# Kernel optimization log

Hardware: AMD Instinct MI355X
Metric: run time of the kernel (lower is better)

Reference implementation:

```python
import jax, jax.numpy as jnp
import numpy as np

# Model constants (match init_kwargs + mamba_ssm defaults)
CIN, COUT, K, STRIDE = 64, 128, 4, 4
D = 128            # d_model = features_out
DI = 256           # d_inner = 2*D (expand=2)
NSTATE = 16        # d_state
DCONV = 4          # depthwise conv width
DT_RANK = 8        # ceil(D/16)
NB = 3             # blocks per direction
NTOT = 2 * NB      # forward + backward stacks


def setup_inputs() -> dict:
    key = jax.random.key(0)
    ks = jax.random.split(key, 10)
    s = 0.02
    x = jax.random.normal(ks[0], (2, CIN, 8192), jnp.float32)
    convd_w = jax.random.normal(ks[1], (COUT, CIN, K), jnp.float32) * s
    convd_b = jnp.zeros((COUT,), jnp.float32)
    ln_w = jnp.ones((NTOT, D), jnp.float32)
    ln_b = jnp.zeros((NTOT, D), jnp.float32)
    in_proj_w = jax.random.normal(ks[2], (NTOT, 2 * DI, D), jnp.float32) * s
    conv_w = jax.random.normal(ks[3], (NTOT, DI, DCONV), jnp.float32) * s
    conv_b = jnp.zeros((NTOT, DI), jnp.float32)
    xproj_w = jax.random.normal(ks[4], (NTOT, DT_RANK + 2 * NSTATE, DI), jnp.float32) * s
    dtproj_w = jax.random.normal(ks[5], (NTOT, DI, DT_RANK), jnp.float32) * s
    dtproj_b = jax.random.normal(ks[6], (NTOT, DI), jnp.float32) * s
    # S4D-real init: A = -[1..N]
    A_log = jnp.log(jnp.broadcast_to(jnp.arange(1, NSTATE + 1, dtype=jnp.float32), (NTOT, DI, NSTATE)))
    Dparam = jnp.ones((NTOT, DI), jnp.float32)
    outproj_w = jax.random.normal(ks[7], (NTOT, D, DI), jnp.float32) * s
    return dict(x=x, convd_w=convd_w, convd_b=convd_b, ln_w=ln_w, ln_b=ln_b,
                in_proj_w=in_proj_w, conv_w=conv_w, conv_b=conv_b, xproj_w=xproj_w,
                dtproj_w=dtproj_w, dtproj_b=dtproj_b, A_log=A_log, Dparam=Dparam,
                outproj_w=outproj_w)


def _silu(x):
    return x * jax.nn.sigmoid(x)


def _layernorm(x, w, b, eps=1e-5):
    m = x.mean(-1, keepdims=True)
    xc = x - m
    v = (xc * xc).mean(-1, keepdims=True)
    return xc * jax.lax.rsqrt(v + eps) * w + b


def _mamba_mixer(x, in_proj_w, conv_w, conv_b, xproj_w, dtproj_w, dtproj_b, A_log, Dp, outproj_w):
    # x: (B, L, D)
    B, L, _ = x.shape
    xz = jnp.einsum('bld,ed->ble', x, in_proj_w)          # (B, L, 2*DI)
    xm, z = jnp.split(xz, 2, axis=-1)
    # causal depthwise conv (pad left DCONV-1, truncate to L)
    xp = jnp.pad(xm, ((0, 0), (DCONV - 1, 0), (0, 0)))
    xc = conv_b
    acc = jnp.zeros_like(xm)
    for k in range(DCONV):
        acc = acc + xp[:, k:k + L, :] * conv_w[:, k]
    xc = _silu(acc + conv_b)                               # (B, L, DI)
    dbc = jnp.einsum('ble,ne->bln', xc, xproj_w)           # (B, L, DT_RANK + 2N)
    dt, Bc, Cc = jnp.split(dbc, [DT_RANK, DT_RANK + NSTATE], axis=-1)
    dt = jax.nn.softplus(jnp.einsum('blr,dr->bld', dt, dtproj_w) + dtproj_b)  # (B, L, DI)
    A = -jnp.exp(A_log)                                    # (DI, N)
    dA = jnp.exp(dt[..., None] * A)                        # (B, L, DI, N)
    dBx = dt[..., None] * Bc[:, :, None, :] * xc[..., None]

    def step(h, inp):
        dA_t, dBx_t, C_t = inp
        h = dA_t * h + dBx_t                               # (B, DI, N)
        y = jnp.einsum('bdn,bn->bd', h, C_t)
        return h, y

    h0 = jnp.zeros((B, DI, NSTATE), x.dtype)
    _, ys = jax.lax.scan(step, h0, (jnp.swapaxes(dA, 0, 1), jnp.swapaxes(dBx, 0, 1), jnp.swapaxes(Cc, 0, 1)))
    y = jnp.swapaxes(ys, 0, 1)                             # (B, L, DI)
    y = (y + Dp * xc) * _silu(z)
    return jnp.einsum('ble,de->bld', y, outproj_w)         # (B, L, D)


def _mamba_stack(x, off, ln_w, ln_b, in_proj_w, conv_w, conv_b, xproj_w, dtproj_w, dtproj_b, A_log, Dparam, outproj_w):
    # mamba_ssm Block semantics: residual = x (+ prev residual); x = mixer(norm(residual))
    res = None
    cur = x
    for i in range(NB):
        j = off + i
        res = cur if res is None else cur + res
        hn = _layernorm(res, ln_w[j], ln_b[j])
        cur = _mamba_mixer(hn, in_proj_w[j], conv_w[j], conv_b[j], xproj_w[j],
                           dtproj_w[j], dtproj_b[j], A_log[j], Dparam[j], outproj_w[j])
    return cur, res


def reference(x, convd_w, convd_b, ln_w, ln_b, in_proj_w, conv_w, conv_b, xproj_w,
              dtproj_w, dtproj_b, A_log, Dparam, outproj_w):
    # downsampling conv + SiLU
    y = jax.lax.conv_general_dilated(x, convd_w, (STRIDE,), 'VALID',
                                     dimension_numbers=('NCH', 'OIH', 'NCH'))
    y = _silu(y + convd_b[None, :, None])                  # (B, COUT, L')
    h = jnp.swapaxes(y, 1, 2)                              # (B, L', D)
    xf, rf = _mamba_stack(h, 0, ln_w, ln_b, in_proj_w, conv_w, conv_b, xproj_w,
                          dtproj_w, dtproj_b, A_log, Dparam, outproj_w)
    xb, rb = _mamba_stack(h[:, ::-1, :], NB, ln_w, ln_b, in_proj_w, conv_w, conv_b, xproj_w,
                          dtproj_w, dtproj_b, A_log, Dparam, outproj_w)
    out = (xf + rf) + (xb + rb)[:, ::-1, :]
    return jnp.swapaxes(out, 1, 2), rf, rb
```

## Files before the change

kernel.cpp:

```cpp
#include <hip/hip_runtime.h>
#include <hip/hip_bf16.h>
#include <math.h>

#define B    2
#define CIN  64
#define LIN  8192
#define L    2048
#define D    128
#define DI   256
#define NS   16
#define RK   8
#define NSTREAM 4
#define CH   32
#define NCH  (L/CH)
#define TOK  (NSTREAM*L)
#define SZ_D ((size_t)TOK*D)
#define SZ_DI ((size_t)TOK*DI)
#define SXM 280
#define SHN 152

typedef short  bfrag __attribute__((ext_vector_type(8)));
typedef float  facc  __attribute__((ext_vector_type(4)));
#define MFMA __builtin_amdgcn_mfma_f32_16x16x32_bf16

__device__ __forceinline__ float sigmoidf_(float x){ return 1.f/(1.f+__expf(-x)); }
__device__ __forceinline__ float siluf_(float x){ return x*sigmoidf_(x); }
__device__ __forceinline__ ushort f2bf(float f){
    unsigned u = __float_as_uint(f);
    u += 0x7fffu + ((u>>16)&1u);
    return (ushort)(u>>16);
}
__device__ __forceinline__ float bf2f(ushort u){ return __uint_as_float(((unsigned)u)<<16); }
__device__ __forceinline__ float softplusf_(float t){
    return (t > 20.f) ? t : __logf(1.f + __expf(t));
}

__global__ void k_cvtall(const float* __restrict__ cw, const float* __restrict__ ipw,
                         const float* __restrict__ opw, const float* __restrict__ xpw,
                         ushort* __restrict__ dst){
    int i = blockIdx.x*256 + threadIdx.x;
    ushort v;
    if (i < 32768)       v = f2bf(cw[i]);
    else if (i < 425984) v = f2bf(ipw[i-32768]);
    else if (i < 622592) v = f2bf(opw[i-425984]);
    else {
        int t = i - 622592;
        int k = t & 255, nr = (t>>8) & 63, j = t>>14;
        v = (nr < 40) ? f2bf(xpw[((size_t)j*40 + nr)*256 + k]) : (ushort)0;
    }
    dst[i] = v;
}

__global__ void k_down(const float* __restrict__ x, const ushort* __restrict__ wd,
                       const float* __restrict__ bias, float* __restrict__ h){
    __shared__ ushort sxd[64*SXM];
    int tid = threadIdx.x;
    int m0 = blockIdx.x*64;
    int b = m0 >> 11;
    int l0 = m0 & 2047;
    for (int idx = tid; idx < 64*64; idx += 256){
        int t = idx & 63, cc = idx >> 6;
        float4 v = *(const float4*)(x + ((size_t)(b*CIN + cc))*LIN + 4*(l0+t));
        ushort4 o; o.x=f2bf(v.x); o.y=f2bf(v.y); o.z=f2bf(v.z); o.w=f2bf(v.w);
        *(ushort4*)&sxd[t*SXM + cc*4] = o;
    }
    __syncthreads();
    int w = tid>>6, lane = tid&63, rw = w>>1, cw = w&1;
    int q = lane>>4, r = lane&15;
    int n0 = blockIdx.y*64 + cw*32;
    const ushort* b0p = wd + (size_t)(n0 + r)*256 + q*8;
    const ushort* b1p = b0p + (size_t)16*256;
    facc acc[2][2] = {};
    #pragma unroll
    for (int kb=0; kb<8; ++kb){
        bfrag a0 = *(bfrag*)&sxd[(rw*32 + r)*SXM + kb*32 + q*8];
        bfrag a1 = *(bfrag*)&sxd[(rw*32 + 16 + r)*SXM + kb*32 + q*8];
        bfrag b0 = *(const bfrag*)(b0p + kb*32);
        bfrag b1 = *(const bfrag*)(b1p + kb*32);
        acc[0][0] = MFMA(a0,b0,acc[0][0],0,0,0);
        acc[0][1] = MFMA(a0,b1,acc[0][1],0,0,0);
        acc[1][0] = MFMA(a1,b0,acc[1][0],0,0,0);
        acc[1][1] = MFMA(a1,b1,acc[1][1],0,0,0);
    }
    #pragma unroll
    for (int im=0; im<2; ++im)
    #pragma unroll
    for (int in=0; in<2; ++in){
        int col = n0 + in*16 + r;
        float bv = bias[col];
        #pragma unroll
        for (int r2=0; r2<4; ++r2){
            int row = m0 + rw*32 + im*16 + q*4 + r2;
            int bb = row >> 11, l = row & 2047;
            float v = siluf_(acc[im][in][r2] + bv);
            h[((size_t)(bb*L + l))*D + col] = v;
            h[((size_t)((2+bb)*L + (L-1-l)))*D + col] = v;
        }
    }
}

__global__ void __launch_bounds__(256,1)
k_head(const float* __restrict__ curIn, const float* __restrict__ resIn,
       float* __restrict__ resOut,
       const float* __restrict__ lnw, const float* __restrict__ lnb,
       const ushort* __restrict__ wbi, const ushort* __restrict__ wbx,
       const float* __restrict__ cw, const float* __restrict__ cb,
       const float* __restrict__ Wdt, const float* __restrict__ bdt,
       const float* __restrict__ A_log,
       float* __restrict__ z, float* __restrict__ xc,
       float* __restrict__ dtr, float* __restrict__ Bc, float* __restrict__ Cc,
       float* __restrict__ Aprod, float* __restrict__ Bend, int blk, int first){
    __shared__ ushort smHn[35*SHN];
    __shared__ ushort smXm[35*SXM];
    __shared__ ushort smXc[32*SXM];
    __shared__ float  smDbc[32*68];
    const int tid = threadIdx.x;
    const int bi = blockIdx.x;
    const int s = bi >> 6, c = bi & 63;
    const int j = (s>>1)*3 + blk;
    const int base_tok = s*L + c*CH;

    {
        int t = tid >> 3, g8 = tid & 7;
        size_t off = (size_t)(base_tok + t)*D + g8*16;
        float4 v[4];
        const float4* cp = (const float4*)(curIn + off);
        #pragma unroll
        for (int i=0;i<4;++i) v[i] = cp[i];
        if (!first){
            const float4* rp = (const float4*)(resIn + off);
            #pragma unroll
            for (int i=0;i<4;++i){ float4 rv=rp[i]; v[i].x+=rv.x; v[i].y+=rv.y; v[i].z+=rv.z; v[i].w+=rv.w; }
        }
        {
            float4* ro = (float4*)(resOut + off);
            #pragma unroll
            for (int i=0;i<4;++i) ro[i] = v[i];
        }
        float s1=0.f, s2=0.f;
        #pragma unroll
        for (int i=0;i<4;++i){
            s1 += v[i].x+v[i].y+v[i].z+v[i].w;
            s2 += v[i].x*v[i].x+v[i].y*v[i].y+v[i].z*v[i].z+v[i].w*v[i].w;
        }
        s1 += __shfl_xor(s1,1); s2 += __shfl_xor(s2,1);
        s1 += __shfl_xor(s1,2); s2 += __shfl_xor(s2,2);
        s1 += __shfl_xor(s1,4); s2 += __shfl_xor(s2,4);
        float mean = s1*(1.f/128.f);
        float var  = s2*(1.f/128.f) - mean*mean;
        float rstd = rsqrtf(var + 1e-5f);
        const float4* lwp = (const float4*)(lnw + j*D + g8*16);
        const float4* lbp = (const float4*)(lnb + j*D + g8*16);
        #pragma unroll
        for (int i=0;i<4;++i){
            float4 lw = lwp[i], lb = lbp[i];
            ushort4 o;
            o.x = f2bf((v[i].x-mean)*rstd*lw.x + lb.x);
            o.y = f2bf((v[i].y-mean)*rstd*lw.y + lb.y);
            o.z = f2bf((v[i].z-mean)*rstd*lw.z + lb.z);
            o.w = f2bf((v[i].w-mean)*rstd*lw.w + lb.w);
            *(ushort4*)&smHn[t*SHN + g8*16 + i*4] = o;
        }
    }
    if (c > 0 && tid < 24){
        int t = tid >> 3, g8 = tid & 7;
        size_t off = (size_t)(base_tok - 3 + t)*D + g8*16;
        float4 v[4];
        const float4* cp = (const float4*)(curIn + off);
        #pragma unroll
        for (int i=0;i<4;++i) v[i] = cp[i];
        if (!first){
            const float4* rp = (const float4*)(resIn + off);
            #pragma unroll
            for (int i=0;i<4;++i){ float4 rv=rp[i]; v[i].x+=rv.x; v[i].y+=rv.y; v[i].z+=rv.z; v[i].w+=rv.w; }
        }
        float s1=0.f, s2=0.f;
        #pragma unroll
        for (int i=0;i<4;++i){
            s1 += v[i].x+v[i].y+v[i].z+v[i].w;
            s2 += v[i].x*v[i].x+v[i].y*v[i].y+v[i].z*v[i].z+v[i].w*v[i].w;
        }
        s1 += __shfl_xor(s1,1); s2 += __shfl_xor(s2,1);
        s1 += __shfl_xor(s1,2); s2 += __shfl_xor(s2,2);
        s1 += __shfl_xor(s1,4); s2 += __shfl_xor(s2,4);
        float mean = s1*(1.f/128.f);
        float var  = s2*(1.f/128.f) - mean*mean;
        float rstd = rsqrtf(var + 1e-5f);
        const float4* lwp = (const float4*)(lnw + j*D + g8*16);
        const float4* lbp = (const float4*)(lnb + j*D + g8*16);
        #pragma unroll
        for (int i=0;i<4;++i){
            float4 lw = lwp[i], lb = lbp[i];
            ushort4 o;
            o.x = f2bf((v[i].x-mean)*rstd*lw.x + lb.x);
            o.y = f2bf((v[i].y-mean)*rstd*lw.y + lb.y);
            o.z = f2bf((v[i].z-mean)*rstd*lw.z + lb.z);
            o.w = f2bf((v[i].w-mean)*rstd*lw.w + lb.w);
            *(ushort4*)&smHn[(32+t)*SHN + g8*16 + i*4] = o;
        }
    }
    __syncthreads();

    {
        int w = tid>>6, lane = tid&63, q = lane>>4, r = lane&15;
        bfrag a[3][4];
        #pragma unroll
        for (int rt=0; rt<3; ++rt)
        #pragma unroll
        for (int kb=0; kb<4; ++kb)
            a[rt][kb] = *(bfrag*)&smHn[(rt*16 + r)*SHN + kb*32 + q*8];
        #pragma unroll
        for (int ct=0; ct<8; ++ct){
            int n0 = w*128 + ct*16;
            const ushort* bp = wbi + ((size_t)j*512 + n0 + r)*128 + q*8;
            facc a0 = {}, a1 = {}, a2 = {};
            #pragma unroll
            for (int kb=0; kb<4; ++kb){
                bfrag bv = *(const bfrag*)(bp + kb*32);
                a0 = MFMA(a[0][kb], bv, a0, 0,0,0);
                a1 = MFMA(a[1][kb], bv, a1, 0,0,0);
                a2 = MFMA(a[2][kb], bv, a2, 0,0,0);
            }
            int colL = n0 + r;
            if (colL < DI){
                #pragma unroll
                for (int r2=0;r2<4;++r2){
                    int rr = q*4 + r2;
                    smXm[rr*SXM + colL]      = f2bf(a0[r2]);
                    smXm[(16+rr)*SXM + colL] = f2bf(a1[r2]);
                    if (rr < 3) smXm[(32+rr)*SXM + colL] = f2bf(a2[r2]);
                }
            } else {
                int cz = colL - DI;
                #pragma unroll
                for (int r2=0;r2<4;++r2){
                    int rr = q*4 + r2;
                    z[(size_t)(base_tok + rr)*DI + cz]      = a0[r2];
                    z[(size_t)(base_tok + 16 + rr)*DI + cz] = a1[r2];
                }
            }
        }
    }
    __syncthreads();

    {
        const float* w4 = cw + ((size_t)j*DI + tid)*4;
        float cw0=w4[0], cw1=w4[1], cw2=w4[2], cw3=w4[3];
        float cbb = cb[j*DI + tid];
        float xm1=0.f, xm2=0.f, xm3=0.f;
        if (c > 0){
            xm3 = bf2f(smXm[32*SXM + tid]);
            xm2 = bf2f(smXm[33*SXM + tid]);
            xm1 = bf2f(smXm[34*SXM + tid]);
        }
        #pragma unroll 4
        for (int i=0;i<CH;++i){
            float x0 = bf2f(smXm[i*SXM + tid]);
            float v = siluf_(cbb + cw3*x0 + cw2*xm1 + cw1*xm2 + cw0*xm3);
            smXc[i*SXM + tid] = f2bf(v);
            xc[(size_t)(base_tok+i)*DI + tid] = v;
            xm3 = xm2; xm2 = xm1; xm1 = x0;
        }
    }
    __syncthreads();

    {
        int w = tid>>6, lane = tid&63, q = lane>>4, r = lane&15;
        facc a0 = {}, a1 = {};
        const ushort* bp = wbx + ((size_t)j*64 + w*16 + r)*256 + q*8;
        #pragma unroll
        for (int kb=0; kb<8; ++kb){
            bfrag av0 = *(bfrag*)&smXc[r*SXM + kb*32 + q*8];
            bfrag av1 = *(bfrag*)&smXc[(16+r)*SXM + kb*32 + q*8];
            bfrag bv  = *(const bfrag*)(bp + kb*32);
            a0 = MFMA(av0, bv, a0, 0,0,0);
            a1 = MFMA(av1, bv, a1, 0,0,0);
        }
        int col = w*16 + r;
        #pragma unroll
        for (int r2=0;r2<4;++r2){
            int rr = q*4 + r2;
            smDbc[rr*68 + col]      = a0[r2];
            smDbc[(16+rr)*68 + col] = a1[r2];
            int row0 = base_tok + rr, row1 = base_tok + 16 + rr;
            if      (col < 8){  dtr[(size_t)row0*RK + col] = a0[r2];      dtr[(size_t)row1*RK + col] = a1[r2]; }
            else if (col < 24){ Bc [(size_t)row0*NS + (col-8)] = a0[r2];  Bc [(size_t)row1*NS + (col-8)] = a1[r2]; }
            else if (col < 40){ Cc [(size_t)row0*NS + (col-24)] = a0[r2]; Cc [(size_t)row1*NS + (col-24)] = a1[r2]; }
        }
    }
    __syncthreads();

    {
        float A[NS], wv[RK];
        const float* ar = A_log + ((size_t)j*DI + tid)*NS;
        #pragma unroll
        for (int n=0;n<NS;++n) A[n] = -__expf(ar[n]);
        const float* wr = Wdt + ((size_t)j*DI + tid)*RK;
        #pragma unroll
        for (int r=0;r<RK;++r) wv[r] = wr[r];
        float bb2 = bdt[j*DI + tid];
        float ap[NS], hs[NS];
        #pragma unroll
        for (int n=0;n<NS;++n){ ap[n]=1.f; hs[n]=0.f; }
        #pragma unroll 4
        for (int l=0;l<CH;++l){
            float t = bb2;
            #pragma unroll
            for (int r=0;r<RK;++r) t += smDbc[l*68+r]*wv[r];
            float dtv = softplusf_(t);
            float xv  = bf2f(smXc[l*SXM + tid]);
            float dbx = dtv*xv;
            #pragma unroll
            for (int n=0;n<NS;++n){
                float dA = __expf(dtv*A[n]);
                ap[n] *= dA;
                hs[n] = dA*hs[n] + dbx*smDbc[l*68+8+n];
            }
        }
        size_t pb = (size_t)bi*4096 + tid;
        #pragma unroll
        for (int n=0;n<NS;++n){
            Aprod[pb + (size_t)n*256] = ap[n];
            Bend [pb + (size_t)n*256] = hs[n];
        }
    }
}

__global__ void k_scanmid(const float* __restrict__ Aprod, float* __restrict__ Bend){
    int tid = blockIdx.x*128 + threadIdx.x;
    int s = tid >> 12;
    int nd = tid & 4095;
    size_t base = (size_t)s*NCH*4096 + nd;
    float h = 0.f;
    for (int c0=0; c0<NCH; c0+=16){
        float a[16], b[16];
        #pragma unroll
        for (int i=0;i<16;++i){
            a[i] = Aprod[base + (size_t)(c0+i)*4096];
            b[i] = Bend [base + (size_t)(c0+i)*4096];
        }
        #pragma unroll
        for (int i=0;i<16;++i){
            Bend[base + (size_t)(c0+i)*4096] = h;
            h = a[i]*h + b[i];
        }
    }
}

__global__ void k_tail(const float* __restrict__ dtr, const float* __restrict__ xcv,
                       const float* __restrict__ Bc, const float* __restrict__ Cc,
                       const float* __restrict__ A_log,
                       const float* __restrict__ Wdt, const float* __restrict__ bdt,
                       const float* __restrict__ h0, const float* __restrict__ z,
                       const float* __restrict__ Dp, const ushort* __restrict__ wbo,
                       float* __restrict__ cur, int blk){
    int c = blockIdx.x, s = blockIdx.y; int j = (s>>1)*3 + blk;
    int d = threadIdx.x;
    __shared__ float sB[CH*NS], sC[CH*NS], sdtr[CH*RK];
    __shared__ ushort sg[CH*SXM];
    int base_tok = s*L + c*CH;
    sB[d] = Bc[(size_t)base_tok*NS + d];
    sB[256+d] = Bc[(size_t)base_tok*NS + 256 + d];
    sC[d] = Cc[(size_t)base_tok*NS + d];
    sC[256+d] = Cc[(size_t)base_tok*NS + 256 + d];
    sdtr[d] = dtr[(size_t)base_tok*RK + d];
    float A[NS], wv[RK];
    const float* ar = A_log + ((size_t)j*DI + d)*NS;
    #pragma unroll
    for (int n=0;n<NS;++n) A[n] = -__expf(ar[n]);
    const float* wr = Wdt + ((size_t)j*DI + d)*RK;
    #pragma unroll
    for (int r=0;r<RK;++r) wv[r] = wr[r];
    float bb = bdt[j*DI + d];
    float Dpd = Dp[j*DI + d];
    float hs[NS];
    size_t pb = (size_t)(s*NCH + c)*4096 + d;
    #pragma unroll
    for (int n=0;n<NS;++n) hs[n] = h0[pb + (size_t)n*256];
    __syncthreads();
    #pragma unroll 4
    for (int l=0;l<CH;++l){
        float t = bb;
        #pragma unroll
        for (int r=0;r<RK;++r) t += sdtr[l*RK+r]*wv[r];
        float dtv = softplusf_(t);
        float xv  = xcv[(size_t)(base_tok+l)*DI + d];
        float dbx = dtv*xv;
        float p = 0.f;
        #pragma unroll
        for (int n=0;n<NS;++n){
            float dA = __expf(dtv*A[n]);
            hs[n] = dA*hs[n] + dbx*sB[l*NS+n];
            p += hs[n]*sC[l*NS+n];
        }
        float zv = z[(size_t)(base_tok+l)*DI + d];
        sg[l*SXM + d] = f2bf((p + Dpd*xv)*siluf_(zv));
    }
    __syncthreads();
    int w = d>>6, lane = d&63, q = lane>>4, r = lane&15;
    facc acc[2][2] = {};
    const ushort* b0p = wbo + ((size_t)j*128 + w*32 + r)*256 + q*8;
    const ushort* b1p = b0p + 16*256;
    #pragma unroll
    for (int kb=0; kb<8; ++kb){
        bfrag av0 = *(bfrag*)&sg[r*SXM + kb*32 + q*8];
        bfrag av1 = *(bfrag*)&sg[(16+r)*SXM + kb*32 + q*8];
        bfrag bv0 = *(const bfrag*)(b0p + kb*32);
        bfrag bv1 = *(const bfrag*)(b1p + kb*32);
        acc[0][0] = MFMA(av0,bv0,acc[0][0],0,0,0);
        acc[0][1] = MFMA(av0,bv1,acc[0][1],0,0,0);
        acc[1][0] = MFMA(av1,bv0,acc[1][0],0,0,0);
        acc[1][1] = MFMA(av1,bv1,acc[1][1],0,0,0);
    }
    #pragma unroll
    for (int rt=0; rt<2; ++rt)
    #pragma unroll
    for (int ct=0; ct<2; ++ct){
        int col = w*32 + ct*16 + r;
        #pragma unroll
        for (int r2=0;r2<4;++r2){
            int row = base_tok + rt*16 + q*4 + r2;
            cur[(size_t)row*D + col] = acc[rt][ct][r2];
        }
    }
}

__global__ void k_final(const float* __restrict__ cur, const float* __restrict__ res,
                        float* __restrict__ out){
    int l = blockIdx.x, b = blockIdx.y, d = threadIdx.x;
    int tf = (b*L + l)*D + d;
    int tbk = ((2+b)*L + (L-1-l))*D + d;
    float f  = cur[tf] + res[tf];
    float bw = cur[tbk] + res[tbk];
    out[((size_t)(b*D + d))*L + l] = f + bw;
    out[(size_t)2*D*L + (size_t)(b*L + l)*D + d] = res[tf];
    out[(size_t)2*D*L + (size_t)((2+b)*L + l)*D + d] = res[((2+b)*L + l)*D + d];
}

extern "C" void kernel_launch(void* const* d_in, const int* in_sizes, int n_in,
                              void* d_out, int out_size, void* d_ws, size_t ws_size,
                              hipStream_t stream){
    const float* x         = (const float*)d_in[0];
    const float* convd_w   = (const float*)d_in[1];
    const float* convd_b   = (const float*)d_in[2];
    const float* ln_w      = (const float*)d_in[3];
    const float* ln_b      = (const float*)d_in[4];
    const float* in_proj_w = (const float*)d_in[5];
    const float* conv_w    = (const float*)d_in[6];
    const float* conv_b    = (const float*)d_in[7];
    const float* xproj_w   = (const float*)d_in[8];
    const float* dtproj_w  = (const float*)d_in[9];
    const float* dtproj_b  = (const float*)d_in[10];
    const float* A_log     = (const float*)d_in[11];
    const float* Dparam    = (const float*)d_in[12];
    const float* outproj_w = (const float*)d_in[13];

    float* ws = (float*)d_ws;
    float* h     = ws; ws += SZ_D;
    float* res0  = ws; ws += SZ_D;
    float* res1  = ws; ws += SZ_D;
    float* cur   = ws; ws += SZ_D;
    float* z     = ws; ws += SZ_DI;
    float* xc    = ws; ws += SZ_DI;
    float* Aprod = ws; ws += SZ_D;
    float* Bend  = ws; ws += SZ_D;
    float* dtr   = ws; ws += (size_t)TOK*RK;
    float* Bc    = ws; ws += (size_t)TOK*NS;
    float* Cc    = ws; ws += (size_t)TOK*NS;
    ushort* wall = (ushort*)ws;
    ushort* wbd  = wall;
    ushort* wbi  = wall + 32768;
    ushort* wbo  = wall + 425984;
    ushort* wbx  = wall + 622592;

    k_cvtall<<<2816, 256, 0, stream>>>(convd_w, in_proj_w, outproj_w, xproj_w, wall);
    k_down<<<dim3(64, 2), 256, 0, stream>>>(x, wbd, convd_b, h);

    float* resin[3]  = { nullptr, res0, res1 };
    float* resout[3] = { res0,    res1, res0 };
    for (int blk = 0; blk < 3; ++blk){
        const float* ci = (blk==0) ? h : cur;
        const float* ri = (blk==0) ? h : resin[blk];
        k_head<<<NSTREAM*NCH, 256, 0, stream>>>(ci, ri, resout[blk], ln_w, ln_b, wbi, wbx,
                                                conv_w, conv_b, dtproj_w, dtproj_b, A_log,
                                                z, xc, dtr, Bc, Cc, Aprod, Bend, blk, blk==0);
        k_scanmid<<<128, 128, 0, stream>>>(Aprod, Bend);
        k_tail<<<dim3(NCH, NSTREAM), 256, 0, stream>>>(dtr, xc, Bc, Cc, A_log,
                                                       dtproj_w, dtproj_b, Bend, z,
                                                       Dparam, wbo, cur, blk);
    }

    k_final<<<dim3(L, B), 128, 0, stream>>>(cur, res0, (float*)d_out);
}
```

Baseline: 254.4 us.

## Store z and xc intermediates as bf16 and tile-transpose final output

```diff
diff --git a/kernel.cpp b/kernel.cpp
--- a/kernel.cpp
+++ b/kernel.cpp
@@ -107,12 +107,11 @@
        const float* __restrict__ cw, const float* __restrict__ cb,
        const float* __restrict__ Wdt, const float* __restrict__ bdt,
        const float* __restrict__ A_log,
-       float* __restrict__ z, float* __restrict__ xc,
+       ushort* __restrict__ zb, ushort* __restrict__ xcb,
        float* __restrict__ dtr, float* __restrict__ Bc, float* __restrict__ Cc,
        float* __restrict__ Aprod, float* __restrict__ Bend, int blk, int first){
     __shared__ ushort smHn[35*SHN];
     __shared__ ushort smXm[35*SXM];
-    __shared__ ushort smXc[32*SXM];
     __shared__ float  smDbc[32*68];
     const int tid = threadIdx.x;
     const int bi = blockIdx.x;
@@ -235,8 +234,8 @@
                 #pragma unroll
                 for (int r2=0;r2<4;++r2){
                     int rr = q*4 + r2;
-                    z[(size_t)(base_tok + rr)*DI + cz]      = a0[r2];
-                    z[(size_t)(base_tok + 16 + rr)*DI + cz] = a1[r2];
+                    zb[(size_t)(base_tok + rr)*DI + cz]      = f2bf(a0[r2]);
+                    zb[(size_t)(base_tok + 16 + rr)*DI + cz] = f2bf(a1[r2]);
                 }
             }
         }
@@ -257,8 +256,9 @@
         for (int i=0;i<CH;++i){
             float x0 = bf2f(smXm[i*SXM + tid]);
             float v = siluf_(cbb + cw3*x0 + cw2*xm1 + cw1*xm2 + cw0*xm3);
-            smXc[i*SXM + tid] = f2bf(v);
-            xc[(size_t)(base_tok+i)*DI + tid] = v;
+            ushort us = f2bf(v);
+            smXm[i*SXM + tid] = us;
+            xcb[(size_t)(base_tok+i)*DI + tid] = us;
             xm3 = xm2; xm2 = xm1; xm1 = x0;
         }
     }
@@ -270,8 +270,8 @@
         const ushort* bp = wbx + ((size_t)j*64 + w*16 + r)*256 + q*8;
         #pragma unroll
         for (int kb=0; kb<8; ++kb){
-            bfrag av0 = *(bfrag*)&smXc[r*SXM + kb*32 + q*8];
-            bfrag av1 = *(bfrag*)&smXc[(16+r)*SXM + kb*32 + q*8];
+            bfrag av0 = *(bfrag*)&smXm[r*SXM + kb*32 + q*8];
+            bfrag av1 = *(bfrag*)&smXm[(16+r)*SXM + kb*32 + q*8];
             bfrag bv  = *(const bfrag*)(bp + kb*32);
             a0 = MFMA(av0, bv, a0, 0,0,0);
             a1 = MFMA(av1, bv, a1, 0,0,0);
@@ -308,7 +308,7 @@
             #pragma unroll
             for (int r=0;r<RK;++r) t += smDbc[l*68+r]*wv[r];
             float dtv = softplusf_(t);
-            float xv  = bf2f(smXc[l*SXM + tid]);
+            float xv  = bf2f(smXm[l*SXM + tid]);
             float dbx = dtv*xv;
             #pragma unroll
             for (int n=0;n<NS;++n){
@@ -347,11 +347,11 @@
     }
 }
 
-__global__ void k_tail(const float* __restrict__ dtr, const float* __restrict__ xcv,
+__global__ void k_tail(const float* __restrict__ dtr, const ushort* __restrict__ xcb,
                        const float* __restrict__ Bc, const float* __restrict__ Cc,
                        const float* __restrict__ A_log,
                        const float* __restrict__ Wdt, const float* __restrict__ bdt,
-                       const float* __restrict__ h0, const float* __restrict__ z,
+                       const float* __restrict__ h0, const ushort* __restrict__ zb,
                        const float* __restrict__ Dp, const ushort* __restrict__ wbo,
                        float* __restrict__ cur, int blk){
     int c = blockIdx.x, s = blockIdx.y; int j = (s>>1)*3 + blk;
@@ -359,11 +359,11 @@
     __shared__ float sB[CH*NS], sC[CH*NS], sdtr[CH*RK];
     __shared__ ushort sg[CH*SXM];
     int base_tok = s*L + c*CH;
-    sB[d] = Bc[(size_t)base_tok*NS + d];
+    sB[d]     = Bc[(size_t)base_tok*NS + d];
     sB[256+d] = Bc[(size_t)base_tok*NS + 256 + d];
-    sC[d] = Cc[(size_t)base_tok*NS + d];
+    sC[d]     = Cc[(size_t)base_tok*NS + d];
     sC[256+d] = Cc[(size_t)base_tok*NS + 256 + d];
-    sdtr[d] = dtr[(size_t)base_tok*RK + d];
+    sdtr[d]   = dtr[(size_t)base_tok*RK + d];
     float A[NS], wv[RK];
     const float* ar = A_log + ((size_t)j*DI + d)*NS;
     #pragma unroll
@@ -384,7 +384,7 @@
         #pragma unroll
         for (int r=0;r<RK;++r) t += sdtr[l*RK+r]*wv[r];
         float dtv = softplusf_(t);
-        float xv  = xcv[(size_t)(base_tok+l)*DI + d];
+        float xv  = bf2f(xcb[(size_t)(base_tok+l)*DI + d]);
         float dbx = dtv*xv;
         float p = 0.f;
         #pragma unroll
@@ -393,7 +393,7 @@
             hs[n] = dA*hs[n] + dbx*sB[l*NS+n];
             p += hs[n]*sC[l*NS+n];
         }
-        float zv = z[(size_t)(base_tok+l)*DI + d];
+        float zv = bf2f(zb[(size_t)(base_tok+l)*DI + d]);
         sg[l*SXM + d] = f2bf((p + Dpd*xv)*siluf_(zv));
     }
     __syncthreads();
@@ -427,14 +427,41 @@
 
 __global__ void k_final(const float* __restrict__ cur, const float* __restrict__ res,
                         float* __restrict__ out){
-    int l = blockIdx.x, b = blockIdx.y, d = threadIdx.x;
-    int tf = (b*L + l)*D + d;
-    int tbk = ((2+b)*L + (L-1-l))*D + d;
-    float f  = cur[tf] + res[tf];
-    float bw = cur[tbk] + res[tbk];
-    out[((size_t)(b*D + d))*L + l] = f + bw;
-    out[(size_t)2*D*L + (size_t)(b*L + l)*D + d] = res[tf];
-    out[(size_t)2*D*L + (size_t)((2+b)*L + l)*D + d] = res[((2+b)*L + l)*D + d];
+    __shared__ float tile[128*33];
+    int tid = threadIdx.x;
+    int c = blockIdx.x, b = blockIdx.y;
+    int t = tid>>3, g8 = tid&7;
+    int lf = c*32 + t, lb = L-1-lf;
+    size_t fo = ((size_t)(b*L + lf))*D + g8*16;
+    size_t bo = ((size_t)((2+b)*L + lb))*D + g8*16;
+    #pragma unroll
+    for (int i=0;i<4;++i){
+        float4 cf  = *(const float4*)(cur + fo + i*4);
+        float4 rf  = *(const float4*)(res + fo + i*4);
+        float4 cb2 = *(const float4*)(cur + bo + i*4);
+        float4 rb2 = *(const float4*)(res + bo + i*4);
+        int db = g8*16 + i*4;
+        tile[(db+0)*33 + t] = cf.x+rf.x+cb2.x+rb2.x;
+        tile[(db+1)*33 + t] = cf.y+rf.y+cb2.y+rb2.y;
+        tile[(db+2)*33 + t] = cf.z+rf.z+cb2.z+rb2.z;
+        tile[(db+3)*33 + t] = cf.w+rf.w+cb2.w+rb2.w;
+    }
+    __syncthreads();
+    int d = tid>>1, hf = tid&1;
+    size_t obase = ((size_t)(b*D + d))*L + c*32 + hf*16;
+    #pragma unroll
+    for (int i=0;i<4;++i){
+        float4 o4;
+        o4.x = tile[d*33 + hf*16 + i*4 + 0];
+        o4.y = tile[d*33 + hf*16 + i*4 + 1];
+        o4.z = tile[d*33 + hf*16 + i*4 + 2];
+        o4.w = tile[d*33 + hf*16 + i*4 + 3];
+        *(float4*)(out + obase + i*4) = o4;
+    }
+    const float4* src = (const float4*)res;
+    float4* dst = (float4*)(out + (size_t)2*D*L);
+    for (int idx = (blockIdx.y*NCH + blockIdx.x)*256 + tid; idx < 262144; idx += 2*NCH*256)
+        dst[idx] = src[idx];
 }
 
 extern "C" void kernel_launch(void* const* d_in, const int* in_sizes, int n_in,
@@ -460,13 +487,13 @@
     float* res0  = ws; ws += SZ_D;
     float* res1  = ws; ws += SZ_D;
     float* cur   = ws; ws += SZ_D;
-    float* z     = ws; ws += SZ_DI;
-    float* xc    = ws; ws += SZ_DI;
     float* Aprod = ws; ws += SZ_D;
     float* Bend  = ws; ws += SZ_D;
     float* dtr   = ws; ws += (size_t)TOK*RK;
     float* Bc    = ws; ws += (size_t)TOK*NS;
     float* Cc    = ws; ws += (size_t)TOK*NS;
+    ushort* zb   = (ushort*)ws; ws += SZ_DI/2;
+    ushort* xcb  = (ushort*)ws; ws += SZ_DI/2;
     ushort* wall = (ushort*)ws;
     ushort* wbd  = wall;
     ushort* wbi  = wall + 32768;
@@ -483,12 +510,12 @@
         const float* ri = (blk==0) ? h : resin[blk];
         k_head<<<NSTREAM*NCH, 256, 0, stream>>>(ci, ri, resout[blk], ln_w, ln_b, wbi, wbx,
                                                 conv_w, conv_b, dtproj_w, dtproj_b, A_log,
-                                                z, xc, dtr, Bc, Cc, Aprod, Bend, blk, blk==0);
+                                                zb, xcb, dtr, Bc, Cc, Aprod, Bend, blk, blk==0);
         k_scanmid<<<128, 128, 0, stream>>>(Aprod, Bend);
-        k_tail<<<dim3(NCH, NSTREAM), 256, 0, stream>>>(dtr, xc, Bc, Cc, A_log,
-                                                       dtproj_w, dtproj_b, Bend, z,
+        k_tail<<<dim3(NCH, NSTREAM), 256, 0, stream>>>(dtr, xcb, Bc, Cc, A_log,
+                                                       dtproj_w, dtproj_b, Bend, zb,
                                                        Dparam, wbo, cur, blk);
     }
 
-    k_final<<<dim3(L, B), 128, 0, stream>>>(cur, res0, (float*)d_out);
-}
+    k_final<<<dim3(NCH, B), 256, 0, stream>>>(cur, res0, (float*)d_out);
+}
```

Result: no change. 258.6 us (+1.7%).
